# Performance work log

Hardware: AMD Instinct MI355X
Metric: run time of the kernel (lower is better)

## Reference

```python
import jax, jax.numpy as jnp
import numpy as np

B, L, D_IN = 2, 4096, 512
H, D_K, D_V, D_OUT = 8, 64, 64, 512


def setup_inputs() -> dict:
    key = jax.random.key(0)
    k0, k1, k2, k3, k4 = jax.random.split(key, 5)
    x = jax.random.normal(k0, (B, L, D_IN), dtype=jnp.float32)
    W_q = jax.random.uniform(k1, (H, D_IN, D_K), dtype=jnp.float32)
    W_k = jax.random.uniform(k2, (H, D_IN, D_K), dtype=jnp.float32)
    W_v = jax.random.uniform(k3, (H, D_IN, D_V), dtype=jnp.float32)
    W_o = jax.random.uniform(k4, (H, D_V, D_OUT), dtype=jnp.float32)
    return {"x": x, "W_q": W_q, "W_k": W_k, "W_v": W_v, "W_o": W_o}


def reference(x, W_q, W_k, W_v, W_o):
    # x: (b, l, d_in); projections per head -> (b, h, l, d)
    Q = jnp.einsum('hjk,blj->bhlk', W_q, x)
    K = jnp.einsum('hjk,blj->bhlk', W_k, x)
    V = jnp.einsum('hjv,blj->bhlv', W_v, x)
    # no softmax: pure bilinear attention (Q K^T) V
    scores = jnp.einsum('bhik,bhjk->bhij', Q, K)          # (b, h, l, l)
    values = jnp.einsum('bhqk,bhkv->bhqv', scores, V)     # (b, h, l, d_v)
    return jnp.einsum('hvo,bhlv->blo', W_o, values)       # (b, l, d_out)
```

## Files before the change

kernel.cpp:

```cpp
#include <hip/hip_runtime.h>
#include <cstdint>


#define BDIM 2
#define LDIM 4096
#define DIN 512
#define HDIM 8
#define DK 64
#define DV 64
#define DOUT 512

using bf16_t = __bf16;
typedef __bf16 bf16x8 __attribute__((ext_vector_type(8)));
typedef float floatx4 __attribute__((ext_vector_type(4)));

__device__ __forceinline__ unsigned short f2bf(float f) {
    unsigned int u = __builtin_bit_cast(unsigned int, f);
    u += 0x7FFFu + ((u >> 16) & 1u);
    return (unsigned short)(u >> 16);
}

__device__ __forceinline__ void gld_lds16(const void* g, void* l) {
    __builtin_amdgcn_global_load_lds(
        (const __attribute__((address_space(1))) void*)g,
        (__attribute__((address_space(3))) void*)l, 16, 0, 0);
}

template <int BM, int BN, int BK, bool TRANS_OUT, int OUT_MODE>
__device__ __forceinline__ void gemm_core(const bf16_t* A, const bf16_t* B,
                                          void* Cp, int K, int lda, int ldb,
                                          int ldc, int tm, int tn) {
    constexpr int WM = BM / 2, WN = BN / 2;
    constexpr int FM = WM / 16, FN = WN / 16;
    constexpr int CPR = BK / 8;
    __shared__ bf16_t As[BM * BK];
    __shared__ bf16_t Bs[BN * BK];
    const int tid = threadIdx.x;
    const int lane = tid & 63;
    const int wr = (tid >> 7) & 1;
    const int wc = (tid >> 6) & 1;

    A += (size_t)tm * lda;
    B += (size_t)tn * ldb;

    floatx4 acc[FM][FN] = {};

    for (int k0 = 0; k0 < K; k0 += BK) {
#pragma unroll
        for (int i = 0; i < (BM * CPR) / 256; ++i) {
            int c = i * 256 + tid;
            int m = c / CPR, kc = c % CPR;
            gld_lds16(A + (size_t)m * lda + k0 + kc * 8, As + c * 8);
        }
#pragma unroll
        for (int i = 0; i < (BN * CPR) / 256; ++i) {
            int c = i * 256 + tid;
            int m = c / CPR, kc = c % CPR;
            gld_lds16(B + (size_t)m * ldb + k0 + kc * 8, Bs + c * 8);
        }
        __syncthreads();

#pragma unroll
        for (int kk = 0; kk < BK; kk += 32) {
            bf16x8 aF[FM], bF[FN];
#pragma unroll
            for (int fm = 0; fm < FM; ++fm)
                aF[fm] = *(const bf16x8*)(As + (wr * WM + fm * 16 + (lane & 15)) * BK +
                                          kk + (lane >> 4) * 8);
#pragma unroll
            for (int fn = 0; fn < FN; ++fn)
                bF[fn] = *(const bf16x8*)(Bs + (wc * WN + fn * 16 + (lane & 15)) * BK +
                                          kk + (lane >> 4) * 8);
#pragma unroll
            for (int fm = 0; fm < FM; ++fm)
#pragma unroll
                for (int fn = 0; fn < FN; ++fn)
                    acc[fm][fn] = __builtin_amdgcn_mfma_f32_16x16x32_bf16(
                        aF[fm], bF[fn], acc[fm][fn], 0, 0, 0);
        }
        __syncthreads();
    }

    const int cr4 = (lane >> 4) * 4;
    const int cn = lane & 15;
#pragma unroll
    for (int fm = 0; fm < FM; ++fm)
#pragma unroll
        for (int fn = 0; fn < FN; ++fn)
#pragma unroll
            for (int r = 0; r < 4; ++r) {
                int m = tm + wr * WM + fm * 16 + cr4 + r;
                int n = tn + wc * WN + fn * 16 + cn;
                size_t idx = TRANS_OUT ? ((size_t)n * ldc + m)
                                       : ((size_t)m * ldc + n);
                if (OUT_MODE == 0)
                    ((float*)Cp)[idx] = acc[fm][fn][r];
                else
                    ((unsigned short*)Cp)[idx] = f2bf(acc[fm][fn][r]);
            }
}

__global__ __launch_bounds__(256) void k_kvm(const bf16_t* xb16,
                                             const bf16_t* WkvT, float* M32) {
    constexpr int EP = 136;
    __shared__ bf16_t smem[128 * EP];
    bf16_t* As = smem;
    bf16_t* Bs = smem + 128 * 64;
    const int lt = blockIdx.x, h = blockIdx.y, b = blockIdx.z;
    const int tid = threadIdx.x;
    const int lane = tid & 63;
    const int wr = (tid >> 7) & 1, wc = (tid >> 6) & 1;
    const int cr4 = (lane >> 4) * 4, cn = lane & 15;

    const bf16_t* A = xb16 + (size_t)b * LDIM * DIN + (size_t)lt * 128 * DIN;
    const bf16_t* B = WkvT + (size_t)h * 128 * DIN;

    floatx4 acc[4][4] = {};
    for (int k0 = 0; k0 < DIN; k0 += 64) {
#pragma unroll
        for (int i = 0; i < 4; ++i) {
            int c = i * 256 + tid, m = c >> 3, kc = c & 7;
            gld_lds16(A + (size_t)m * DIN + k0 + kc * 8, As + c * 8);
        }
#pragma unroll
        for (int i = 0; i < 4; ++i) {
            int c = i * 256 + tid, m = c >> 3, kc = c & 7;
            gld_lds16(B + (size_t)m * DIN + k0 + kc * 8, Bs + c * 8);
        }
        __syncthreads();
#pragma unroll
        for (int kk = 0; kk < 64; kk += 32) {
            bf16x8 aF[4], bF[4];
#pragma unroll
            for (int fm = 0; fm < 4; ++fm)
                aF[fm] = *(const bf16x8*)(As + (wr * 64 + fm * 16 + cn) * 64 +
                                          kk + (lane >> 4) * 8);
#pragma unroll
            for (int fn = 0; fn < 4; ++fn)
                bF[fn] = *(const bf16x8*)(Bs + (wc * 64 + fn * 16 + cn) * 64 +
                                          kk + (lane >> 4) * 8);
#pragma unroll
            for (int fm = 0; fm < 4; ++fm)
#pragma unroll
                for (int fn = 0; fn < 4; ++fn)
                    acc[fm][fn] = __builtin_amdgcn_mfma_f32_16x16x32_bf16(
                        aF[fm], bF[fn], acc[fm][fn], 0, 0, 0);
        }
        __syncthreads();
    }

#pragma unroll
    for (int fm = 0; fm < 4; ++fm)
#pragma unroll
        for (int fn = 0; fn < 4; ++fn)
#pragma unroll
            for (int r = 0; r < 4; ++r) {
                int m = wr * 64 + fm * 16 + cr4 + r;
                int n = wc * 64 + fn * 16 + cn;
                ((unsigned short*)smem)[n * EP + m] = f2bf(acc[fm][fn][r]);
            }
    __syncthreads();

    floatx4 mm[2][2] = {};
#pragma unroll
    for (int kk = 0; kk < 128; kk += 32) {
        bf16x8 aF[2], bF[2];
#pragma unroll
        for (int f = 0; f < 2; ++f) {
            aF[f] = *(const bf16x8*)(smem + (wr * 32 + f * 16 + cn) * EP + kk +
                                     (lane >> 4) * 8);
            bF[f] = *(const bf16x8*)(smem + (64 + wc * 32 + f * 16 + cn) * EP +
                                     kk + (lane >> 4) * 8);
        }
#pragma unroll
        for (int fm = 0; fm < 2; ++fm)
#pragma unroll
            for (int fn = 0; fn < 2; ++fn)
                mm[fm][fn] = __builtin_amdgcn_mfma_f32_16x16x32_bf16(
                    aF[fm], bF[fn], mm[fm][fn], 0, 0, 0);
    }
    float* Mh = M32 + ((size_t)(b * HDIM + h)) * (DK * DV);
#pragma unroll
    for (int fm = 0; fm < 2; ++fm)
#pragma unroll
        for (int fn = 0; fn < 2; ++fn)
#pragma unroll
            for (int r = 0; r < 4; ++r) {
                int dk = wr * 32 + fm * 16 + cr4 + r;
                int v = wc * 32 + fn * 16 + cn;
                atomicAdd(&Mh[dk * 64 + v], mm[fm][fn][r]);
            }
}

__global__ __launch_bounds__(256) void k_tail(const bf16_t* WqC, const bf16_t* WoT,
                                              const float* M32, unsigned short* CT) {
    int i0 = blockIdx.x * 64, o0 = blockIdx.y * 64, b = blockIdx.z;
    __shared__ bf16_t Aq[64 * 64];
    __shared__ bf16_t Ws[64 * 64];
    __shared__ bf16_t Msh[64 * 64];
    __shared__ bf16_t PTs[64 * 64];
    const int tid = threadIdx.x;
    const int lane = tid & 63;
    const int wr = (tid >> 7) & 1, wc = (tid >> 6) & 1;
    const int cr4 = (lane >> 4) * 4, cn = lane & 15;

    floatx4 acc[2][2] = {};

    for (int h = 0; h < HDIM; ++h) {
#pragma unroll
        for (int i = 0; i < 2; ++i) {
            int c = i * 256 + tid, m = c >> 3, kc = c & 7;
            gld_lds16(WqC + (size_t)(i0 + m) * DIN + h * 64 + kc * 8, Aq + c * 8);
            gld_lds16(WoT + ((size_t)h * DOUT + o0 + m) * DV + kc * 8, Ws + c * 8);
        }
        const float* Mh = M32 + ((size_t)(b * HDIM + h)) * (DK * DV);
#pragma unroll
        for (int i = 0; i < 4; ++i) {
            int idx = (i * 256 + tid) * 4;
            float4 v = *(const float4*)(Mh + idx);
            *(ushort4*)((unsigned short*)Msh + idx) =
                make_ushort4(f2bf(v.x), f2bf(v.y), f2bf(v.z), f2bf(v.w));
        }
        __syncthreads();

        floatx4 pt[2][2] = {};
#pragma unroll
        for (int kk = 0; kk < 64; kk += 32) {
            bf16x8 aF[2], bF[2];
#pragma unroll
            for (int f = 0; f < 2; ++f) {
                aF[f] = *(const bf16x8*)(Ws + (wr * 32 + f * 16 + cn) * 64 + kk +
                                         (lane >> 4) * 8);
                bF[f] = *(const bf16x8*)(Msh + (wc * 32 + f * 16 + cn) * 64 + kk +
                                         (lane >> 4) * 8);
            }
#pragma unroll
            for (int fm = 0; fm < 2; ++fm)
#pragma unroll
                for (int fn = 0; fn < 2; ++fn)
                    pt[fm][fn] = __builtin_amdgcn_mfma_f32_16x16x32_bf16(
                        aF[fm], bF[fn], pt[fm][fn], 0, 0, 0);
        }
#pragma unroll
        for (int fm = 0; fm < 2; ++fm)
#pragma unroll
            for (int fn = 0; fn < 2; ++fn)
#pragma unroll
                for (int r = 0; r < 4; ++r) {
                    int m = wr * 32 + fm * 16 + cr4 + r;
                    int n = wc * 32 + fn * 16 + cn;
                    ((unsigned short*)PTs)[m * 64 + n] = f2bf(pt[fm][fn][r]);
                }
        __syncthreads();

#pragma unroll
        for (int kk = 0; kk < 64; kk += 32) {
            bf16x8 aF[2], bF[2];
#pragma unroll
            for (int f = 0; f < 2; ++f) {
                aF[f] = *(const bf16x8*)(PTs + (wr * 32 + f * 16 + cn) * 64 + kk +
                                         (lane >> 4) * 8);
                bF[f] = *(const bf16x8*)(Aq + (wc * 32 + f * 16 + cn) * 64 + kk +
                                         (lane >> 4) * 8);
            }
#pragma unroll
            for (int fm = 0; fm < 2; ++fm)
#pragma unroll
                for (int fn = 0; fn < 2; ++fn)
                    acc[fm][fn] = __builtin_amdgcn_mfma_f32_16x16x32_bf16(
                        aF[fm], bF[fn], acc[fm][fn], 0, 0, 0);
        }
        __syncthreads();
    }

    unsigned short* CTb = CT + (size_t)b * DIN * DOUT;
#pragma unroll
    for (int fm = 0; fm < 2; ++fm)
#pragma unroll
        for (int fn = 0; fn < 2; ++fn)
#pragma unroll
            for (int r = 0; r < 4; ++r) {
                int m = wr * 32 + fm * 16 + cr4 + r;
                int n = wc * 32 + fn * 16 + cn;
                CTb[(size_t)(o0 + m) * DIN + i0 + n] = f2bf(acc[fm][fn][r]);
            }
}

__global__ __launch_bounds__(256) void k_out(const bf16_t* x16, const bf16_t* CT,
                                             float* out) {
    int b = blockIdx.z;
    gemm_core<64, 128, 64, false, 0>(x16 + (size_t)b * LDIM * DIN,
                                     CT + (size_t)b * DIN * DOUT,
                                     out + (size_t)b * LDIM * DOUT, DIN, DIN,
                                     DIN, DOUT, blockIdx.x * 64,
                                     blockIdx.y * 128);
}

__global__ __launch_bounds__(256) void k_prep2(
    const float* x, const float* Wq, const float* Wk, const float* Wv,
    const float* Wo, unsigned short* xb, unsigned short* WqC,
    unsigned short* WkvT, unsigned short* WoT, float* M32) {
    __shared__ unsigned short T[64][65];
    int tr = threadIdx.x >> 4, tc4 = (threadIdx.x & 15) * 4;
    int bid = blockIdx.x;
    if (bid < 2048) {
        size_t base = ((size_t)bid * 256 + threadIdx.x) * 8;
        float4 v0 = *(const float4*)(x + base);
        float4 v1 = *(const float4*)(x + base + 4);
        unsigned short o[8] = {f2bf(v0.x), f2bf(v0.y), f2bf(v0.z), f2bf(v0.w),
                               f2bf(v1.x), f2bf(v1.y), f2bf(v1.z), f2bf(v1.w)};
        *(uint4*)(xb + base) = *(const uint4*)o;
        return;
    }
    if (bid >= 2304) {
        size_t g = ((size_t)(bid - 2304) * 256 + threadIdx.x) * 32;
        float4 z4 = make_float4(0.f, 0.f, 0.f, 0.f);
#pragma unroll
        for (int q = 0; q < 8; ++q) *(float4*)(M32 + g + q * 4) = z4;
        return;
    }
    int p_ = bid - 2048;
    int t = p_ & 7, job = (p_ >> 3) & 3, h = p_ >> 5;
    if (job == 0) {
        const float* src = Wq + (size_t)h * DIN * DK;
#pragma unroll
        for (int p = 0; p < 4; ++p) {
            int i = t * 64 + p * 16 + tr;
            float4 v = *(const float4*)(src + (size_t)i * DK + tc4);
            *(ushort4*)(WqC + (size_t)i * (HDIM * DK) + h * DK + tc4) =
                make_ushort4(f2bf(v.x), f2bf(v.y), f2bf(v.z), f2bf(v.w));
        }
        return;
    }
    const float* src;
    unsigned short* dst;
    int rows, cols, r0, c0;
    if (job == 1) {
        src = Wk + (size_t)h * DIN * DK;
        dst = WkvT + ((size_t)h * 128) * DIN;
        rows = DIN; cols = DK; r0 = t * 64; c0 = 0;
    } else if (job == 2) {
        src = Wv + (size_t)h * DIN * DV;
        dst = WkvT + ((size_t)h * 128 + 64) * DIN;
        rows = DIN; cols = DV; r0 = t * 64; c0 = 0;
    } else {
        src = Wo + (size_t)h * DV * DOUT;
        dst = WoT + (size_t)h * DOUT * DV;
        rows = DV; cols = DOUT; r0 = 0; c0 = t * 64;
    }
#pragma unroll
    for (int p = 0; p < 4; ++p) {
        int r = p * 16 + tr;
        float4 v = *(const float4*)(src + (size_t)(r0 + r) * cols + c0 + tc4);
        T[r][tc4 + 0] = f2bf(v.x); T[r][tc4 + 1] = f2bf(v.y);
        T[r][tc4 + 2] = f2bf(v.z); T[r][tc4 + 3] = f2bf(v.w);
    }
    __syncthreads();
#pragma unroll
    for (int p = 0; p < 4; ++p) {
        int c = p * 16 + tr;
        ushort4 u = make_ushort4(T[tc4 + 0][c], T[tc4 + 1][c], T[tc4 + 2][c],
                                 T[tc4 + 3][c]);
        *(ushort4*)(dst + (size_t)(c0 + c) * rows + r0 + tc4) = u;
    }
}

extern "C" void kernel_launch(void* const* d_in, const int* in_sizes, int n_in,
                              void* d_out, int out_size, void* d_ws, size_t ws_size,
                              hipStream_t stream) {
    const float* x  = (const float*)d_in[0];
    const float* Wq = (const float*)d_in[1];
    const float* Wk = (const float*)d_in[2];
    const float* Wv = (const float*)d_in[3];
    const float* Wo = (const float*)d_in[4];
    float* out = (float*)d_out;

    unsigned short* w = (unsigned short*)d_ws;
    unsigned short* xb16  = w; w += (size_t)BDIM * LDIM * DIN;
    unsigned short* WqC   = w; w += (size_t)DIN * HDIM * DK;
    unsigned short* WkvT  = w; w += (size_t)1024 * DIN;
    unsigned short* WoT   = w; w += (size_t)HDIM * DOUT * DV;
    unsigned short* CT    = w; w += (size_t)BDIM * DIN * DOUT;
    float* M32 = (float*)(((uintptr_t)w + 255) & ~(uintptr_t)255);

    k_prep2<<<dim3(2312), 256, 0, stream>>>(x, Wq, Wk, Wv, Wo, xb16, WqC,
                                            WkvT, WoT, M32);
    k_kvm<<<dim3(LDIM / 128, HDIM, BDIM), 256, 0, stream>>>(
        (const bf16_t*)xb16, (const bf16_t*)WkvT, M32);
    k_tail<<<dim3(8, 8, BDIM), 256, 0, stream>>>((const bf16_t*)WqC,
                                                 (const bf16_t*)WoT, M32, CT);
    k_out<<<dim3(LDIM / 64, DOUT / 128, BDIM), 256, 0, stream>>>(
        (const bf16_t*)xb16, (const bf16_t*)CT, out);
}
```

Before: 124.6 us.

## Compute per-head K^T V via shared Gram matrix X^T X

```diff
diff --git a/kernel.cpp b/kernel.cpp
--- a/kernel.cpp
+++ b/kernel.cpp
@@ -33,8 +33,8 @@
     constexpr int WM = BM / 2, WN = BN / 2;
     constexpr int FM = WM / 16, FN = WN / 16;
     constexpr int CPR = BK / 8;
-    __shared__ bf16_t As[BM * BK];
-    __shared__ bf16_t Bs[BN * BK];
+    __shared__ __align__(16) bf16_t As[BM * BK];
+    __shared__ __align__(16) bf16_t Bs[BN * BK];
     const int tid = threadIdx.x;
     const int lane = tid & 63;
     const int wr = (tid >> 7) & 1;
@@ -95,110 +95,104 @@
                                        : ((size_t)m * ldc + n);
                 if (OUT_MODE == 0)
                     ((float*)Cp)[idx] = acc[fm][fn][r];
+                else if (OUT_MODE == 1)
+                    ((unsigned short*)Cp)[idx] = f2bf(acc[fm][fn][r]);
                 else
-                    ((unsigned short*)Cp)[idx] = f2bf(acc[fm][fn][r]);
-            }
-}
-
-__global__ __launch_bounds__(256) void k_kvm(const bf16_t* xb16,
-                                             const bf16_t* WkvT, float* M32) {
-    constexpr int EP = 136;
-    __shared__ bf16_t smem[128 * EP];
-    bf16_t* As = smem;
-    bf16_t* Bs = smem + 128 * 64;
-    const int lt = blockIdx.x, h = blockIdx.y, b = blockIdx.z;
+                    atomicAdd((float*)Cp + idx, acc[fm][fn][r]);
+            }
+}
+
+__global__ __launch_bounds__(256) void k_xtx(const bf16_t* xT, float* G32) {
+    const int t = blockIdx.x;
+    const int chunk = blockIdx.y;
+    const int b = blockIdx.z;
+    const int i0 = (t >> 3) * 128, j0 = (t & 7) * 64;
+    const bf16_t* Xb = xT + (size_t)b * DIN * LDIM + (size_t)chunk * 512;
+    gemm_core<128, 64, 64, false, 2>(Xb, Xb, G32 + (size_t)b * DIN * DIN, 512,
+                                     LDIM, LDIM, DIN, i0, j0);
+}
+
+__global__ __launch_bounds__(256) void k_gv(const bf16_t* WkT, const float* G32,
+                                            unsigned short* T2) {
+    const int jt = blockIdx.x, h = blockIdx.y, b = blockIdx.z;
+    const int j0 = jt * 64;
+    __shared__ __align__(16) bf16_t As[64 * 64];
+    __shared__ __align__(16) bf16_t Bs[64 * 64];
     const int tid = threadIdx.x;
     const int lane = tid & 63;
     const int wr = (tid >> 7) & 1, wc = (tid >> 6) & 1;
     const int cr4 = (lane >> 4) * 4, cn = lane & 15;
 
-    const bf16_t* A = xb16 + (size_t)b * LDIM * DIN + (size_t)lt * 128 * DIN;
-    const bf16_t* B = WkvT + (size_t)h * 128 * DIN;
-
-    floatx4 acc[4][4] = {};
+    const bf16_t* A = WkT + (size_t)h * DK * DIN;
+    const float* Gb = G32 + (size_t)b * DIN * DIN + (size_t)j0 * DIN;
+
+    floatx4 acc[2][2] = {};
     for (int k0 = 0; k0 < DIN; k0 += 64) {
 #pragma unroll
-        for (int i = 0; i < 4; ++i) {
+        for (int i = 0; i < 2; ++i) {
             int c = i * 256 + tid, m = c >> 3, kc = c & 7;
             gld_lds16(A + (size_t)m * DIN + k0 + kc * 8, As + c * 8);
         }
 #pragma unroll
-        for (int i = 0; i < 4; ++i) {
-            int c = i * 256 + tid, m = c >> 3, kc = c & 7;
-            gld_lds16(B + (size_t)m * DIN + k0 + kc * 8, Bs + c * 8);
+        for (int i = 0; i < 2; ++i) {
+            int c = i * 256 + tid, n = c >> 3, kc = c & 7;
+            const float* src = Gb + (size_t)n * DIN + k0 + kc * 8;
+            float4 v0 = *(const float4*)src;
+            float4 v1 = *(const float4*)(src + 4);
+            unsigned short o[8] = {f2bf(v0.x), f2bf(v0.y), f2bf(v0.z), f2bf(v0.w),
+                                   f2bf(v1.x), f2bf(v1.y), f2bf(v1.z), f2bf(v1.w)};
+            *(uint4*)((unsigned short*)Bs + (size_t)c * 8) = *(const uint4*)o;
         }
         __syncthreads();
 #pragma unroll
         for (int kk = 0; kk < 64; kk += 32) {
-            bf16x8 aF[4], bF[4];
-#pragma unroll
-            for (int fm = 0; fm < 4; ++fm)
-                aF[fm] = *(const bf16x8*)(As + (wr * 64 + fm * 16 + cn) * 64 +
-                                          kk + (lane >> 4) * 8);
-#pragma unroll
-            for (int fn = 0; fn < 4; ++fn)
-                bF[fn] = *(const bf16x8*)(Bs + (wc * 64 + fn * 16 + cn) * 64 +
-                                          kk + (lane >> 4) * 8);
-#pragma unroll
-            for (int fm = 0; fm < 4; ++fm)
-#pragma unroll
-                for (int fn = 0; fn < 4; ++fn)
+            bf16x8 aF[2], bF[2];
+#pragma unroll
+            for (int f = 0; f < 2; ++f) {
+                aF[f] = *(const bf16x8*)(As + (wr * 32 + f * 16 + cn) * 64 + kk +
+                                         (lane >> 4) * 8);
+                bF[f] = *(const bf16x8*)(Bs + (wc * 32 + f * 16 + cn) * 64 + kk +
+                                         (lane >> 4) * 8);
+            }
+#pragma unroll
+            for (int fm = 0; fm < 2; ++fm)
+#pragma unroll
+                for (int fn = 0; fn < 2; ++fn)
                     acc[fm][fn] = __builtin_amdgcn_mfma_f32_16x16x32_bf16(
                         aF[fm], bF[fn], acc[fm][fn], 0, 0, 0);
         }
         __syncthreads();
     }
 
-#pragma unroll
-    for (int fm = 0; fm < 4; ++fm)
-#pragma unroll
-        for (int fn = 0; fn < 4; ++fn)
+    unsigned short* dst = T2 + (size_t)(b * HDIM + h) * DK * DIN;
+#pragma unroll
+    for (int fm = 0; fm < 2; ++fm)
+#pragma unroll
+        for (int fn = 0; fn < 2; ++fn)
 #pragma unroll
             for (int r = 0; r < 4; ++r) {
-                int m = wr * 64 + fm * 16 + cr4 + r;
-                int n = wc * 64 + fn * 16 + cn;
-                ((unsigned short*)smem)[n * EP + m] = f2bf(acc[fm][fn][r]);
-            }
-    __syncthreads();
-
-    floatx4 mm[2][2] = {};
-#pragma unroll
-    for (int kk = 0; kk < 128; kk += 32) {
-        bf16x8 aF[2], bF[2];
-#pragma unroll
-        for (int f = 0; f < 2; ++f) {
-            aF[f] = *(const bf16x8*)(smem + (wr * 32 + f * 16 + cn) * EP + kk +
-                                     (lane >> 4) * 8);
-            bF[f] = *(const bf16x8*)(smem + (64 + wc * 32 + f * 16 + cn) * EP +
-                                     kk + (lane >> 4) * 8);
-        }
-#pragma unroll
-        for (int fm = 0; fm < 2; ++fm)
-#pragma unroll
-            for (int fn = 0; fn < 2; ++fn)
-                mm[fm][fn] = __builtin_amdgcn_mfma_f32_16x16x32_bf16(
-                    aF[fm], bF[fn], mm[fm][fn], 0, 0, 0);
-    }
-    float* Mh = M32 + ((size_t)(b * HDIM + h)) * (DK * DV);
-#pragma unroll
-    for (int fm = 0; fm < 2; ++fm)
-#pragma unroll
-        for (int fn = 0; fn < 2; ++fn)
-#pragma unroll
-            for (int r = 0; r < 4; ++r) {
-                int dk = wr * 32 + fm * 16 + cr4 + r;
-                int v = wc * 32 + fn * 16 + cn;
-                atomicAdd(&Mh[dk * 64 + v], mm[fm][fn][r]);
-            }
+                int m = wr * 32 + fm * 16 + cr4 + r;
+                int n = wc * 32 + fn * 16 + cn;
+                dst[(size_t)m * DIN + j0 + n] = f2bf(acc[fm][fn][r]);
+            }
+}
+
+__global__ __launch_bounds__(256) void k_m(const bf16_t* T2, const bf16_t* WvT,
+                                           float* M32) {
+    const int h = blockIdx.x, b = blockIdx.y;
+    gemm_core<64, 64, 64, false, 0>(T2 + (size_t)(b * HDIM + h) * DK * DIN,
+                                    WvT + (size_t)h * DV * DIN,
+                                    M32 + (size_t)(b * HDIM + h) * (DK * DV),
+                                    DIN, DIN, DIN, DV, 0, 0);
 }
 
 __global__ __launch_bounds__(256) void k_tail(const bf16_t* WqC, const bf16_t* WoT,
                                               const float* M32, unsigned short* CT) {
     int i0 = blockIdx.x * 64, o0 = blockIdx.y * 64, b = blockIdx.z;
-    __shared__ bf16_t Aq[64 * 64];
-    __shared__ bf16_t Ws[64 * 64];
-    __shared__ bf16_t Msh[64 * 64];
-    __shared__ bf16_t PTs[64 * 64];
+    __shared__ __align__(16) bf16_t Aq[64 * 64];
+    __shared__ __align__(16) bf16_t Ws[64 * 64];
+    __shared__ __align__(16) bf16_t Msh[64 * 64];
+    __shared__ __align__(16) bf16_t PTs[64 * 64];
     const int tid = threadIdx.x;
     const int lane = tid & 63;
     const int wr = (tid >> 7) & 1, wc = (tid >> 6) & 1;
@@ -296,10 +290,11 @@
                                      blockIdx.y * 128);
 }
 
-__global__ __launch_bounds__(256) void k_prep2(
+__global__ __launch_bounds__(256) void k_prep3(
     const float* x, const float* Wq, const float* Wk, const float* Wv,
-    const float* Wo, unsigned short* xb, unsigned short* WqC,
-    unsigned short* WkvT, unsigned short* WoT, float* M32) {
+    const float* Wo, unsigned short* xb, unsigned short* xT,
+    unsigned short* WqC, unsigned short* WkT, unsigned short* WvT,
+    unsigned short* WoT, float* G32) {
     __shared__ unsigned short T[64][65];
     int tr = threadIdx.x >> 4, tc4 = (threadIdx.x & 15) * 4;
     int bid = blockIdx.x;
@@ -312,14 +307,40 @@
         *(uint4*)(xb + base) = *(const uint4*)o;
         return;
     }
-    if (bid >= 2304) {
-        size_t g = ((size_t)(bid - 2304) * 256 + threadIdx.x) * 32;
+    if (bid < 3072) {
+        int p_ = bid - 2048;
+        int b = p_ >> 9;
+        int q = p_ & 511;
+        int lt = q >> 3, it = q & 7;
+        const float* src = x + (size_t)b * LDIM * DIN + (size_t)lt * 64 * DIN +
+                           (size_t)it * 64;
+        unsigned short* dst = xT + (size_t)b * DIN * LDIM +
+                              (size_t)it * 64 * LDIM + (size_t)lt * 64;
+#pragma unroll
+        for (int p = 0; p < 4; ++p) {
+            int r = p * 16 + tr;
+            float4 v = *(const float4*)(src + (size_t)r * DIN + tc4);
+            T[r][tc4 + 0] = f2bf(v.x); T[r][tc4 + 1] = f2bf(v.y);
+            T[r][tc4 + 2] = f2bf(v.z); T[r][tc4 + 3] = f2bf(v.w);
+        }
+        __syncthreads();
+#pragma unroll
+        for (int p = 0; p < 4; ++p) {
+            int c = p * 16 + tr;
+            ushort4 u = make_ushort4(T[tc4 + 0][c], T[tc4 + 1][c], T[tc4 + 2][c],
+                                     T[tc4 + 3][c]);
+            *(ushort4*)(dst + (size_t)c * LDIM + tc4) = u;
+        }
+        return;
+    }
+    if (bid >= 3328) {
+        size_t g = ((size_t)(bid - 3328) * 256 + threadIdx.x) * 32;
         float4 z4 = make_float4(0.f, 0.f, 0.f, 0.f);
 #pragma unroll
-        for (int q = 0; q < 8; ++q) *(float4*)(M32 + g + q * 4) = z4;
+        for (int q = 0; q < 8; ++q) *(float4*)(G32 + g + q * 4) = z4;
         return;
     }
-    int p_ = bid - 2048;
+    int p_ = bid - 3072;
     int t = p_ & 7, job = (p_ >> 3) & 3, h = p_ >> 5;
     if (job == 0) {
         const float* src = Wq + (size_t)h * DIN * DK;
@@ -337,11 +358,11 @@
     int rows, cols, r0, c0;
     if (job == 1) {
         src = Wk + (size_t)h * DIN * DK;
-        dst = WkvT + ((size_t)h * 128) * DIN;
+        dst = WkT + (size_t)h * DK * DIN;
         rows = DIN; cols = DK; r0 = t * 64; c0 = 0;
     } else if (job == 2) {
         src = Wv + (size_t)h * DIN * DV;
-        dst = WkvT + ((size_t)h * 128 + 64) * DIN;
+        dst = WvT + (size_t)h * DV * DIN;
         rows = DIN; cols = DV; r0 = t * 64; c0 = 0;
     } else {
         src = Wo + (size_t)h * DV * DOUT;
@@ -376,17 +397,23 @@
     float* out = (float*)d_out;
 
     unsigned short* w = (unsigned short*)d_ws;
-    unsigned short* xb16  = w; w += (size_t)BDIM * LDIM * DIN;
-    unsigned short* WqC   = w; w += (size_t)DIN * HDIM * DK;
-    unsigned short* WkvT  = w; w += (size_t)1024 * DIN;
-    unsigned short* WoT   = w; w += (size_t)HDIM * DOUT * DV;
-    unsigned short* CT    = w; w += (size_t)BDIM * DIN * DOUT;
-    float* M32 = (float*)(((uintptr_t)w + 255) & ~(uintptr_t)255);
-
-    k_prep2<<<dim3(2312), 256, 0, stream>>>(x, Wq, Wk, Wv, Wo, xb16, WqC,
-                                            WkvT, WoT, M32);
-    k_kvm<<<dim3(LDIM / 128, HDIM, BDIM), 256, 0, stream>>>(
-        (const bf16_t*)xb16, (const bf16_t*)WkvT, M32);
+    unsigned short* xb16 = w; w += (size_t)BDIM * LDIM * DIN;
+    unsigned short* xT16 = w; w += (size_t)BDIM * DIN * LDIM;
+    unsigned short* WqC  = w; w += (size_t)DIN * HDIM * DK;
+    unsigned short* WkT  = w; w += (size_t)HDIM * DK * DIN;
+    unsigned short* WvT  = w; w += (size_t)HDIM * DV * DIN;
+    unsigned short* WoT  = w; w += (size_t)HDIM * DOUT * DV;
+    unsigned short* CT   = w; w += (size_t)BDIM * DIN * DOUT;
+    unsigned short* T2   = w; w += (size_t)BDIM * HDIM * DK * DIN;
+    float* G32 = (float*)(((uintptr_t)w + 255) & ~(uintptr_t)255);
+    float* M32 = G32 + (size_t)BDIM * DIN * DIN;
+
+    k_prep3<<<dim3(3392), 256, 0, stream>>>(x, Wq, Wk, Wv, Wo, xb16, xT16,
+                                            WqC, WkT, WvT, WoT, G32);
+    k_xtx<<<dim3(32, 8, BDIM), 256, 0, stream>>>((const bf16_t*)xT16, G32);
+    k_gv<<<dim3(8, HDIM, BDIM), 256, 0, stream>>>((const bf16_t*)WkT, G32, T2);
+    k_m<<<dim3(HDIM, BDIM), 256, 0, stream>>>((const bf16_t*)T2,
+                                              (const bf16_t*)WvT, M32);
     k_tail<<<dim3(8, 8, BDIM), 256, 0, stream>>>((const bf16_t*)WqC,
                                                  (const bf16_t*)WoT, M32, CT);
     k_out<<<dim3(LDIM / 64, DOUT / 128, BDIM), 256, 0, stream>>>(
```

Result: slower. 145.8 us (+17.0%).
